# Performance work log

Hardware: AMD Instinct MI355X
Metric: run time of the kernel (lower is better)

Reference implementation:

```python
import jax, jax.numpy as jnp
import numpy as np

DIM = 256
BATCH = 4096
DT = 0.05
T_START, T_END = 0.0, 5.0


def setup_inputs() -> dict:
    key = jax.random.key(0)
    k1, k2 = jax.random.split(key)
    initial_position = jax.random.normal(k1, (BATCH, DIM), dtype=jnp.float32)
    # Parameter A initialized to -I (per module) plus small perturbation so it is not trivially diagonal.
    A = -jnp.eye(DIM, dtype=jnp.float32) + 0.01 * jax.random.normal(k2, (DIM, DIM), dtype=jnp.float32)
    return {"initial_position": initial_position, "A": A}


def reference(initial_position, A):
    # t_values = arange(t_start, t_end, dt) -> T = 100 steps
    t_values = jnp.arange(T_START, T_END, DT, dtype=A.dtype)
    # exp(t * A) for every timestep, batched over t: [T, D, D]
    exp_tA = jax.vmap(lambda t: jax.scipy.linalg.expm(t * A))(t_values)
    # trajectory[b, t, k] = sum_d x0[b, d] * exp_tA[t, k, d]  (x0 @ exp_tA.T per timestep)
    trajectory = jnp.einsum('bd,tkd->btk', initial_position, exp_tA)
    return trajectory
```

## Files before the change

kernel.cpp:

```cpp
#include <hip/hip_runtime.h>
#include <cstdint>
#include <cstddef>


#define TSTEPS 100
#define NCOLS  (TSTEPS * 256)
#define DT     0.05f

typedef _Float16 half8 __attribute__((ext_vector_type(8)));
typedef _Float16 half4 __attribute__((ext_vector_type(4)));
typedef float    f32x4 __attribute__((ext_vector_type(4)));

__global__ void init_kernel(const float* __restrict__ A, float* __restrict__ E0,
                            float* __restrict__ R, float c) {
  int i = blockIdx.x * 256 + threadIdx.x;
  float id = ((i >> 8) == (i & 255)) ? 1.f : 0.f;
  E0[i] = id;
  R[i]  = id + c * A[i];
}

__global__ __launch_bounds__(256) void mm256(const float* __restrict__ A,
                                             const float* __restrict__ Bb,
                                             float* __restrict__ Cb,
                                             float alpha, int addI) {
  const float* B = Bb + (size_t)blockIdx.y * 65536;
  float*       C = Cb + (size_t)blockIdx.y * 65536;
  const int tm = (blockIdx.x & 3) * 64;
  const int tn = (blockIdx.x >> 2) * 64;
  __shared__ float As[64][33];
  __shared__ float Bs[32][68];
  const int t  = threadIdx.x;
  const int tr = t >> 4, tc = t & 15;
  const int arow = t >> 3, acol = (t & 7) * 4;
  const int brow = t >> 4, bcol = (t & 15) * 4;
  float acc[4][4] = {};
  for (int kk = 0; kk < 256; kk += 32) {
    __syncthreads();
#pragma unroll
    for (int p = 0; p < 2; ++p) {
      int r = arow + p * 32;
      const float4 v = *(const float4*)(A + (size_t)(tm + r) * 256 + kk + acol);
      As[r][acol] = v.x; As[r][acol + 1] = v.y; As[r][acol + 2] = v.z; As[r][acol + 3] = v.w;
    }
#pragma unroll
    for (int p = 0; p < 2; ++p) {
      int r = brow + p * 16;
      const float4 v = *(const float4*)(B + (size_t)(kk + r) * 256 + tn + bcol);
      *(float4*)(&Bs[r][bcol]) = v;
    }
    __syncthreads();
#pragma unroll
    for (int k2 = 0; k2 < 32; ++k2) {
      float a0 = As[tr * 4 + 0][k2];
      float a1 = As[tr * 4 + 1][k2];
      float a2 = As[tr * 4 + 2][k2];
      float a3 = As[tr * 4 + 3][k2];
      const float4 b = *(const float4*)(&Bs[k2][tc * 4]);
      acc[0][0] += a0 * b.x; acc[0][1] += a0 * b.y; acc[0][2] += a0 * b.z; acc[0][3] += a0 * b.w;
      acc[1][0] += a1 * b.x; acc[1][1] += a1 * b.y; acc[1][2] += a1 * b.z; acc[1][3] += a1 * b.w;
      acc[2][0] += a2 * b.x; acc[2][1] += a2 * b.y; acc[2][2] += a2 * b.z; acc[2][3] += a2 * b.w;
      acc[3][0] += a3 * b.x; acc[3][1] += a3 * b.y; acc[3][2] += a3 * b.z; acc[3][3] += a3 * b.w;
    }
  }
#pragma unroll
  for (int i = 0; i < 4; ++i) {
    int m = tm + tr * 4 + i;
#pragma unroll
    for (int j = 0; j < 4; ++j) {
      int n = tn + tc * 4 + j;
      float v = alpha * acc[i][j];
      if (addI && m == n) v += 1.f;
      C[(size_t)m * 256 + n] = v;
    }
  }
}

__global__ void f2h(const float* __restrict__ s, _Float16* __restrict__ d) {
  int i = (blockIdx.x * 256 + threadIdx.x) * 4;
  const float4 v = *(const float4*)(s + i);
  half4 h;
  h[0] = (_Float16)v.x; h[1] = (_Float16)v.y; h[2] = (_Float16)v.z; h[3] = (_Float16)v.w;
  *(half4*)(d + i) = h;
}

__global__ __launch_bounds__(256) void gemm_out(const _Float16* __restrict__ X,
                                                const _Float16* __restrict__ W,
                                                float* __restrict__ out) {
  const int bt = blockIdx.x & 31;
  const int nt = blockIdx.x >> 5;
  const int m0 = bt * 128, n0 = nt * 128;
  __shared__ _Float16 As[128 * 72];
  __shared__ _Float16 Bs[128 * 72];
  const int t    = threadIdx.x;
  const int srow = t >> 3;
  const int scol = (t & 7) * 8;
  const int lane = t & 63, wave = t >> 6;
  const int wm = (wave & 1) * 64, wn = (wave >> 1) * 64;
  const int quad = lane >> 4, l16 = lane & 15;

  f32x4 acc[4][4];
#pragma unroll
  for (int i = 0; i < 4; ++i)
#pragma unroll
    for (int j = 0; j < 4; ++j) acc[i][j] = f32x4{0.f, 0.f, 0.f, 0.f};

  for (int kk = 0; kk < 256; kk += 64) {
    __syncthreads();
#pragma unroll
    for (int p = 0; p < 4; ++p) {
      int r = srow + p * 32;
      *(uint4*)(&As[r * 72 + scol]) = *(const uint4*)(X + (size_t)(m0 + r) * 256 + kk + scol);
      *(uint4*)(&Bs[r * 72 + scol]) = *(const uint4*)(W + (size_t)(n0 + r) * 256 + kk + scol);
    }
    __syncthreads();
#pragma unroll
    for (int ks = 0; ks < 64; ks += 32) {
      half8 af[4], bf[4];
#pragma unroll
      for (int i = 0; i < 4; ++i)
        af[i] = *(const half8*)(&As[(wm + i * 16 + l16) * 72 + ks + quad * 8]);
#pragma unroll
      for (int j = 0; j < 4; ++j)
        bf[j] = *(const half8*)(&Bs[(wn + j * 16 + l16) * 72 + ks + quad * 8]);
#pragma unroll
      for (int i = 0; i < 4; ++i)
#pragma unroll
        for (int j = 0; j < 4; ++j)
          acc[i][j] = __builtin_amdgcn_mfma_f32_16x16x32_f16(af[i], bf[j], acc[i][j], 0, 0, 0);
    }
  }
#pragma unroll
  for (int i = 0; i < 4; ++i)
#pragma unroll
    for (int j = 0; j < 4; ++j) {
      const int col = n0 + wn + j * 16 + l16;
#pragma unroll
      for (int r = 0; r < 4; ++r) {
        const int row = m0 + wm + i * 16 + quad * 4 + r;
        out[(size_t)row * NCOLS + col] = acc[i][j][r];
      }
    }
}

extern "C" void kernel_launch(void* const* d_in, const int* in_sizes, int n_in,
                              void* d_out, int out_size, void* d_ws, size_t ws_size,
                              hipStream_t stream) {
  const float* X0 = (const float*)d_in[0];
  const float* A  = (const float*)d_in[1];
  float* out = (float*)d_out;

  float* E  = (float*)d_ws;
  float* R0 = E + (size_t)TSTEPS * 65536;
  float* R1 = R0 + 65536;
  _Float16* Xh = (_Float16*)(R1 + 65536);
  _Float16* Wh = Xh + (size_t)4096 * 256;

  init_kernel<<<256, 256, 0, stream>>>(A, E, R0, DT / 6.f);
  mm256<<<dim3(16, 1), 256, 0, stream>>>(A, R0, R1, DT / 5.f, 1);
  mm256<<<dim3(16, 1), 256, 0, stream>>>(A, R1, R0, DT / 4.f, 1);
  mm256<<<dim3(16, 1), 256, 0, stream>>>(A, R0, R1, DT / 3.f, 1);
  mm256<<<dim3(16, 1), 256, 0, stream>>>(A, R1, R0, DT / 2.f, 1);
  mm256<<<dim3(16, 1), 256, 0, stream>>>(A, R0, E + 65536, DT, 1);
  for (int j = 0; j < 7; ++j) {
    int p   = 1 << j;
    int cnt = (TSTEPS - 1 - p < p) ? (TSTEPS - 1 - p) : p;
    mm256<<<dim3(16, cnt), 256, 0, stream>>>(E + (size_t)p * 65536, E + 65536,
                                             E + (size_t)(p + 1) * 65536, 1.f, 0);
  }

  f2h<<<1024, 256, 0, stream>>>(X0, Xh);
  f2h<<<6400, 256, 0, stream>>>(E, Wh);

  gemm_out<<<32 * 200, 256, 0, stream>>>(Xh, Wh, out);
}
```

Before: 726.0 us.

## Fuse fp16 conversion into matrix powers, drop Taylor term, swizzle LDS loads

The fp16 copy of each exp(tA) matrix is now written straight from the mm256 epilogue, which removes the separate f2h pass over all 100 matrices. The Taylor series for exp(dt*A) is cut by one term, saving a launch at some accuracy cost. mm256 stores A transposed in shared memory so it can use float4 reads, and writes its output with float4 stores. gemm_out switches to direct global-to-LDS loads with an XOR-swizzled layout instead of padding, and remaps block indices to improve L2 locality.

After: 678.9 us. 1.07x faster.

```diff
diff --git a/kernel.cpp b/kernel.cpp
--- a/kernel.cpp
+++ b/kernel.cpp
@@ -11,66 +11,80 @@
 typedef _Float16 half4 __attribute__((ext_vector_type(4)));
 typedef float    f32x4 __attribute__((ext_vector_type(4)));
 
-__global__ void init_kernel(const float* __restrict__ A, float* __restrict__ E0,
-                            float* __restrict__ R, float c) {
+__device__ __forceinline__ void gload16(const _Float16* g, _Float16* l) {
+  __builtin_amdgcn_global_load_lds(
+      (const __attribute__((address_space(1))) void*)g,
+      (__attribute__((address_space(3))) void*)l, 16, 0, 0);
+}
+
+__global__ void init_kernel(const float* __restrict__ A, float* __restrict__ R,
+                            _Float16* __restrict__ Wh0, float c) {
   int i = blockIdx.x * 256 + threadIdx.x;
   float id = ((i >> 8) == (i & 255)) ? 1.f : 0.f;
-  E0[i] = id;
   R[i]  = id + c * A[i];
+  Wh0[i] = (_Float16)id;
 }
 
 __global__ __launch_bounds__(256) void mm256(const float* __restrict__ A,
                                              const float* __restrict__ Bb,
                                              float* __restrict__ Cb,
+                                             _Float16* __restrict__ Hb,
                                              float alpha, int addI) {
   const float* B = Bb + (size_t)blockIdx.y * 65536;
   float*       C = Cb + (size_t)blockIdx.y * 65536;
   const int tm = (blockIdx.x & 3) * 64;
   const int tn = (blockIdx.x >> 2) * 64;
-  __shared__ float As[64][33];
+  __shared__ float Ats[32][68];
   __shared__ float Bs[32][68];
   const int t  = threadIdx.x;
   const int tr = t >> 4, tc = t & 15;
-  const int arow = t >> 3, acol = (t & 7) * 4;
-  const int brow = t >> 4, bcol = (t & 15) * 4;
+  const int am = t >> 3, ak = (t & 7) * 4;
+  const int bk = t >> 4, bn = (t & 15) * 4;
   float acc[4][4] = {};
   for (int kk = 0; kk < 256; kk += 32) {
     __syncthreads();
 #pragma unroll
     for (int p = 0; p < 2; ++p) {
-      int r = arow + p * 32;
-      const float4 v = *(const float4*)(A + (size_t)(tm + r) * 256 + kk + acol);
-      As[r][acol] = v.x; As[r][acol + 1] = v.y; As[r][acol + 2] = v.z; As[r][acol + 3] = v.w;
+      const int m = am + p * 32;
+      const float4 v = *(const float4*)(A + (size_t)(tm + m) * 256 + kk + ak);
+      Ats[ak + 0][m] = v.x; Ats[ak + 1][m] = v.y;
+      Ats[ak + 2][m] = v.z; Ats[ak + 3][m] = v.w;
     }
 #pragma unroll
     for (int p = 0; p < 2; ++p) {
-      int r = brow + p * 16;
-      const float4 v = *(const float4*)(B + (size_t)(kk + r) * 256 + tn + bcol);
-      *(float4*)(&Bs[r][bcol]) = v;
+      const int k = bk + p * 16;
+      *(float4*)(&Bs[k][bn]) = *(const float4*)(B + (size_t)(kk + k) * 256 + tn + bn);
     }
     __syncthreads();
 #pragma unroll
     for (int k2 = 0; k2 < 32; ++k2) {
-      float a0 = As[tr * 4 + 0][k2];
-      float a1 = As[tr * 4 + 1][k2];
-      float a2 = As[tr * 4 + 2][k2];
-      float a3 = As[tr * 4 + 3][k2];
+      const float4 a = *(const float4*)(&Ats[k2][tr * 4]);
       const float4 b = *(const float4*)(&Bs[k2][tc * 4]);
-      acc[0][0] += a0 * b.x; acc[0][1] += a0 * b.y; acc[0][2] += a0 * b.z; acc[0][3] += a0 * b.w;
-      acc[1][0] += a1 * b.x; acc[1][1] += a1 * b.y; acc[1][2] += a1 * b.z; acc[1][3] += a1 * b.w;
-      acc[2][0] += a2 * b.x; acc[2][1] += a2 * b.y; acc[2][2] += a2 * b.z; acc[2][3] += a2 * b.w;
-      acc[3][0] += a3 * b.x; acc[3][1] += a3 * b.y; acc[3][2] += a3 * b.z; acc[3][3] += a3 * b.w;
+      acc[0][0] += a.x * b.x; acc[0][1] += a.x * b.y; acc[0][2] += a.x * b.z; acc[0][3] += a.x * b.w;
+      acc[1][0] += a.y * b.x; acc[1][1] += a.y * b.y; acc[1][2] += a.y * b.z; acc[1][3] += a.y * b.w;
+      acc[2][0] += a.z * b.x; acc[2][1] += a.z * b.y; acc[2][2] += a.z * b.z; acc[2][3] += a.z * b.w;
+      acc[3][0] += a.w * b.x; acc[3][1] += a.w * b.y; acc[3][2] += a.w * b.z; acc[3][3] += a.w * b.w;
     }
   }
+  const int n0c = tn + tc * 4;
 #pragma unroll
   for (int i = 0; i < 4; ++i) {
-    int m = tm + tr * 4 + i;
-#pragma unroll
-    for (int j = 0; j < 4; ++j) {
-      int n = tn + tc * 4 + j;
-      float v = alpha * acc[i][j];
-      if (addI && m == n) v += 1.f;
-      C[(size_t)m * 256 + n] = v;
+    const int m = tm + tr * 4 + i;
+    float4 v;
+    v.x = alpha * acc[i][0]; v.y = alpha * acc[i][1];
+    v.z = alpha * acc[i][2]; v.w = alpha * acc[i][3];
+    if (addI) {
+      const int d = m - n0c;
+      if (d == 0) v.x += 1.f; else if (d == 1) v.y += 1.f;
+      else if (d == 2) v.z += 1.f; else if (d == 3) v.w += 1.f;
+    }
+    *(float4*)(&C[(size_t)m * 256 + n0c]) = v;
+    if (Hb) {
+      _Float16* H = Hb + (size_t)blockIdx.y * 65536;
+      half4 h;
+      h[0] = (_Float16)v.x; h[1] = (_Float16)v.y;
+      h[2] = (_Float16)v.z; h[3] = (_Float16)v.w;
+      *(half4*)(&H[(size_t)m * 256 + n0c]) = h;
     }
   }
 }
@@ -86,17 +100,18 @@
 __global__ __launch_bounds__(256) void gemm_out(const _Float16* __restrict__ X,
                                                 const _Float16* __restrict__ W,
                                                 float* __restrict__ out) {
-  const int bt = blockIdx.x & 31;
-  const int nt = blockIdx.x >> 5;
+  const int nb = (blockIdx.x & 7) * 800 + (blockIdx.x >> 3);
+  const int bt = nb & 31;
+  const int nt = nb >> 5;
   const int m0 = bt * 128, n0 = nt * 128;
-  __shared__ _Float16 As[128 * 72];
-  __shared__ _Float16 Bs[128 * 72];
+  __shared__ __attribute__((aligned(16))) _Float16 As[128 * 64];
+  __shared__ __attribute__((aligned(16))) _Float16 Bs[128 * 64];
   const int t    = threadIdx.x;
-  const int srow = t >> 3;
-  const int scol = (t & 7) * 8;
   const int lane = t & 63, wave = t >> 6;
   const int wm = (wave & 1) * 64, wn = (wave >> 1) * 64;
   const int quad = lane >> 4, l16 = lane & 15;
+  const int srow = lane >> 3;
+  const int gcol = (((lane & 7) ^ srow) << 3);
 
   f32x4 acc[4][4];
 #pragma unroll
@@ -108,20 +123,22 @@
     __syncthreads();
 #pragma unroll
     for (int p = 0; p < 4; ++p) {
-      int r = srow + p * 32;
-      *(uint4*)(&As[r * 72 + scol]) = *(const uint4*)(X + (size_t)(m0 + r) * 256 + kk + scol);
-      *(uint4*)(&Bs[r * 72 + scol]) = *(const uint4*)(W + (size_t)(n0 + r) * 256 + kk + scol);
+      const int rb = wave * 32 + p * 8;
+      const int r  = rb + srow;
+      gload16(X + (size_t)(m0 + r) * 256 + kk + gcol, &As[rb * 64]);
+      gload16(W + (size_t)(n0 + r) * 256 + kk + gcol, &Bs[rb * 64]);
     }
     __syncthreads();
 #pragma unroll
     for (int ks = 0; ks < 64; ks += 32) {
       half8 af[4], bf[4];
+      const int ch = ((ks >> 3) + quad) ^ (l16 & 7);
 #pragma unroll
       for (int i = 0; i < 4; ++i)
-        af[i] = *(const half8*)(&As[(wm + i * 16 + l16) * 72 + ks + quad * 8]);
+        af[i] = *(const half8*)(&As[(wm + i * 16 + l16) * 64 + (ch << 3)]);
 #pragma unroll
       for (int j = 0; j < 4; ++j)
-        bf[j] = *(const half8*)(&Bs[(wn + j * 16 + l16) * 72 + ks + quad * 8]);
+        bf[j] = *(const half8*)(&Bs[(wn + j * 16 + l16) * 64 + (ch << 3)]);
 #pragma unroll
       for (int i = 0; i < 4; ++i)
 #pragma unroll
@@ -155,21 +172,20 @@
   _Float16* Xh = (_Float16*)(R1 + 65536);
   _Float16* Wh = Xh + (size_t)4096 * 256;
 
-  init_kernel<<<256, 256, 0, stream>>>(A, E, R0, DT / 6.f);
-  mm256<<<dim3(16, 1), 256, 0, stream>>>(A, R0, R1, DT / 5.f, 1);
-  mm256<<<dim3(16, 1), 256, 0, stream>>>(A, R1, R0, DT / 4.f, 1);
-  mm256<<<dim3(16, 1), 256, 0, stream>>>(A, R0, R1, DT / 3.f, 1);
-  mm256<<<dim3(16, 1), 256, 0, stream>>>(A, R1, R0, DT / 2.f, 1);
-  mm256<<<dim3(16, 1), 256, 0, stream>>>(A, R0, E + 65536, DT, 1);
+  init_kernel<<<256, 256, 0, stream>>>(A, R0, Wh, DT / 5.f);
+  mm256<<<dim3(16, 1), 256, 0, stream>>>(A, R0, R1, nullptr, DT / 4.f, 1);
+  mm256<<<dim3(16, 1), 256, 0, stream>>>(A, R1, R0, nullptr, DT / 3.f, 1);
+  mm256<<<dim3(16, 1), 256, 0, stream>>>(A, R0, R1, nullptr, DT / 2.f, 1);
+  mm256<<<dim3(16, 1), 256, 0, stream>>>(A, R1, E + 65536, Wh + 65536, DT, 1);
   for (int j = 0; j < 7; ++j) {
     int p   = 1 << j;
     int cnt = (TSTEPS - 1 - p < p) ? (TSTEPS - 1 - p) : p;
     mm256<<<dim3(16, cnt), 256, 0, stream>>>(E + (size_t)p * 65536, E + 65536,
-                                             E + (size_t)(p + 1) * 65536, 1.f, 0);
+                                             E + (size_t)(p + 1) * 65536,
+                                             Wh + (size_t)(p + 1) * 65536, 1.f, 0);
   }
 
   f2h<<<1024, 256, 0, stream>>>(X0, Xh);
-  f2h<<<6400, 256, 0, stream>>>(E, Wh);
 
   gemm_out<<<32 * 200, 256, 0, stream>>>(Xh, Wh, out);
 }
```
